# Optimization experiments

Measured on AMD Instinct MI355X. Metric: run time of the kernel, lower is better.

The kernel has to match this reference:

```python
import jax, jax.numpy as jnp
import numpy as np

NEIGHBOR_K = 3

def setup_inputs() -> dict:
    key = jax.random.key(0)
    k1, k2 = jax.random.split(key)
    query_fea = jax.random.normal(k1, (8, 75, 121, 640), dtype=jnp.float32)
    support_fea = jax.random.normal(k2, (8, 5, 5, 121, 640), dtype=jnp.float32)
    return {"query_fea": query_fea, "support_fea": support_fea}

def reference(query_fea, support_fea):
    # query_fea: [b, n_wq, patch_num, dim]
    # support_fea: [b, way, shot, patch_num, dim]
    b, way, shot, pn, dim = support_fea.shape
    sup = support_fea.reshape(b, way, shot * pn, dim)  # [b, way, S, dim]
    # inner products between every query patch and every support patch
    # sim: [b, n_wq, way, patch_num, S]
    sim = jnp.einsum('bqpd,bwsd->bqwps', query_fea, sup)
    # top-k over support patches (last axis), then mean over all topk values
    topk = jax.lax.top_k(sim, NEIGHBOR_K)[0]  # [b, n_wq, way, patch_num, k]
    return jnp.mean(topk, axis=(-2, -1))  # [b, n_wq, way]
```

## Files before the change

kernel.cpp:

```cpp
#include <hip/hip_runtime.h>
#include <hip/hip_bf16.h>

#define BATCH 8
#define NQ    75
#define WAY   5
#define PN    121
#define DIM   640
#define SSZ   605
#define TOPK  3

#define KCH 10
#define NCH 5

#define NQTILES 6000
#define NSTILES 2000
#define WSQ_BYTES ((size_t)NQTILES * 16384)
#define WS_NEED   ((size_t)(NQTILES + NSTILES) * 16384)

typedef __attribute__((ext_vector_type(8))) short   short8;
typedef __attribute__((ext_vector_type(8))) __bf16  bf16x8;
typedef __attribute__((ext_vector_type(4))) float   f32x4;

__device__ inline unsigned short f2bf(float f) {
  unsigned u = __builtin_bit_cast(unsigned, f);
  return (unsigned short)((u + 0x7fffu + ((u >> 16) & 1u)) >> 16);
}
__device__ inline unsigned pk2(float lo, float hi) {
  return (unsigned)f2bf(lo) | ((unsigned)f2bf(hi) << 16);
}

__device__ inline void ins3(float &a, float &b, float &c, float v) {
  float na  = fmaxf(a, v);
  float nb  = __builtin_amdgcn_fmed3f(v, a, b);
  float nc2 = __builtin_amdgcn_fmed3f(v, b, c);
  a = na; b = nb; c = nc2;
}

__device__ inline void async_copy16(const void* g, void* l) {
  __builtin_amdgcn_global_load_lds(
      (const __attribute__((address_space(1))) unsigned int*)g,
      (__attribute__((address_space(3))) unsigned int*)l, 16, 0, 0);
}

__global__ __launch_bounds__(256) void cvt_pack(const float* __restrict__ qf,
                                                const float* __restrict__ sf,
                                                uint4* __restrict__ wq,
                                                uint4* __restrict__ wsp) {
  const int blk = blockIdx.x;
  const float* src;
  uint4* dstbase;
  int nrows;
  int rowbase;
  if (blk < 1200) {
    const int slab = blk >> 1;
    rowbase = (blk & 1) << 6;
    src = qf + (size_t)slab * PN * DIM;
    dstbase = wq + (size_t)slab * KCH * 1024;
    nrows = PN;
  } else {
    const int u  = blk - 1200;
    const int uv = u >> 1;
    rowbase = (u & 1) << 6;
    const int nc = uv % NCH;
    const int bw = uv / NCH;
    src = sf + ((size_t)bw * SSZ + nc * 128) * DIM;
    dstbase = wsp + (size_t)uv * KCH * 1024;
    nrows = SSZ - nc * 128; if (nrows > 128) nrows = 128;
  }
  #pragma unroll 4
  for (int i = 0; i < 20; ++i) {
    const int L    = i * 256 + threadIdx.x;
    const int rowl = L / 80;
    const int s    = L - rowl * 80;
    const int row  = rowbase + rowl;
    const int kc   = s >> 3;
    const int c    = s & 7;
    const int p    = c ^ (row & 7);
    uint4 o = make_uint4(0u, 0u, 0u, 0u);
    if (row < nrows) {
      const float* g = src + (size_t)row * DIM + s * 8;
      float4 v0 = reinterpret_cast<const float4*>(g)[0];
      float4 v1 = reinterpret_cast<const float4*>(g)[1];
      o.x = pk2(v0.x, v0.y); o.y = pk2(v0.z, v0.w);
      o.z = pk2(v1.x, v1.y); o.w = pk2(v1.z, v1.w);
    }
    dstbase[(size_t)kc * 1024 + row * 8 + p] = o;
  }
}

__global__ __launch_bounds__(256, 3) void lpc_main(
    const char* __restrict__ wq,
    const char* __restrict__ wsp,
    float* __restrict__ out)
{
  __shared__ char Qs[16384];
  __shared__ char Ss[16384];
  __shared__ float red[4];

  const int sbid = blockIdx.x;
  const int bid  = (sbid & 7) * (NQ * WAY) + (sbid >> 3);

  const int w   = bid % WAY;
  const int bq  = bid / WAY;
  const int b   = bid / (WAY * NQ);

  const char* Qtiles = wq  + (size_t)bq * KCH * 16384;
  const char* Stiles = wsp + (size_t)(b * WAY + w) * NCH * KCH * 16384;

  const int tid  = threadIdx.x;
  const int lane = tid & 63;
  const int wv   = tid >> 6;
  const int l15  = lane & 15;
  const int quad = lane >> 4;
  const int mrow0 = (wv >> 1) * 64;
  const int ncol0 = (wv & 1) * 64;

  const int sw16 = (l15 & 7) * 16;
  const int cp0  = (quad * 16) ^ sw16;
  const int cp1  = ((4 + quad) * 16) ^ sw16;

  const char* qb = Qs + (mrow0 + l15) * 128;
  const char* sb = Ss + (ncol0 + l15) * 128;

  float t3a[4][4], t3b[4][4], t3c[4][4];
  #pragma unroll
  for (int mt = 0; mt < 4; ++mt)
    #pragma unroll
    for (int r = 0; r < 4; ++r) {
      t3a[mt][r] = -3.0e38f; t3b[mt][r] = -3.0e38f; t3c[mt][r] = -3.0e38f;
    }

  for (int nc = 0; nc < NCH; ++nc) {
    f32x4 acc[4][4];
    #pragma unroll
    for (int mt = 0; mt < 4; ++mt)
      #pragma unroll
      for (int nt = 0; nt < 4; ++nt)
        acc[mt][nt] = (f32x4){0.f, 0.f, 0.f, 0.f};

    #pragma unroll 1
    for (int kc = 0; kc < KCH; ++kc) {
      __syncthreads();
      {
        const char* qsl = Qtiles + (size_t)kc * 16384;
        const char* ssl = Stiles + ((size_t)nc * KCH + kc) * 16384;
        #pragma unroll
        for (int i = 0; i < 4; ++i) {
          int ch = wv * 4 + i;
          async_copy16(qsl + ch * 1024 + lane * 16, Qs + ch * 1024);
          async_copy16(ssl + ch * 1024 + lane * 16, Ss + ch * 1024);
        }
      }
      __syncthreads();

      #pragma unroll
      for (int kk = 0; kk < 2; ++kk) {
        const int cp = kk ? cp1 : cp0;
        short8 a[4], bf[4];
        #pragma unroll
        for (int mt = 0; mt < 4; ++mt)
          a[mt] = *reinterpret_cast<const short8*>(qb + mt * 2048 + cp);
        #pragma unroll
        for (int nt = 0; nt < 4; ++nt)
          bf[nt] = *reinterpret_cast<const short8*>(sb + nt * 2048 + cp);
        #pragma unroll
        for (int mt = 0; mt < 4; ++mt)
          #pragma unroll
          for (int nt = 0; nt < 4; ++nt)
            acc[mt][nt] = __builtin_amdgcn_mfma_f32_16x16x32_bf16(
                __builtin_bit_cast(bf16x8, a[mt]),
                __builtin_bit_cast(bf16x8, bf[nt]), acc[mt][nt], 0, 0, 0);
      }
    }

    #pragma unroll
    for (int nt = 0; nt < 4; ++nt) {
      int col = nc * 128 + ncol0 + nt * 16 + l15;
      bool valid = col < SSZ;
      #pragma unroll
      for (int mt = 0; mt < 4; ++mt)
        #pragma unroll
        for (int r = 0; r < 4; ++r) {
          float v = valid ? acc[mt][nt][r] : -3.0e38f;
          ins3(t3a[mt][r], t3b[mt][r], t3c[mt][r], v);
        }
    }
  }

  #pragma unroll
  for (int m = 1; m < 16; m <<= 1) {
    #pragma unroll
    for (int mt = 0; mt < 4; ++mt)
      #pragma unroll
      for (int r = 0; r < 4; ++r) {
        float o0 = __shfl_xor(t3a[mt][r], m);
        float o1 = __shfl_xor(t3b[mt][r], m);
        float o2 = __shfl_xor(t3c[mt][r], m);
        ins3(t3a[mt][r], t3b[mt][r], t3c[mt][r], o0);
        ins3(t3a[mt][r], t3b[mt][r], t3c[mt][r], o1);
        ins3(t3a[mt][r], t3b[mt][r], t3c[mt][r], o2);
      }
  }

  float* tb = reinterpret_cast<float*>(Qs);
  __syncthreads();
  if ((wv & 1) == 1 && l15 == 0) {
    #pragma unroll
    for (int mt = 0; mt < 4; ++mt)
      #pragma unroll
      for (int r = 0; r < 4; ++r) {
        int row = mrow0 + mt * 16 + quad * 4 + r;
        tb[row * 3 + 0] = t3a[mt][r];
        tb[row * 3 + 1] = t3b[mt][r];
        tb[row * 3 + 2] = t3c[mt][r];
      }
  }
  __syncthreads();
  if ((wv & 1) == 0 && l15 == 0) {
    #pragma unroll
    for (int mt = 0; mt < 4; ++mt)
      #pragma unroll
      for (int r = 0; r < 4; ++r) {
        int row = mrow0 + mt * 16 + quad * 4 + r;
        ins3(t3a[mt][r], t3b[mt][r], t3c[mt][r], tb[row * 3 + 0]);
        ins3(t3a[mt][r], t3b[mt][r], t3c[mt][r], tb[row * 3 + 1]);
        ins3(t3a[mt][r], t3b[mt][r], t3c[mt][r], tb[row * 3 + 2]);
      }
  }
  __syncthreads();
  if ((wv & 1) == 0 && l15 == 0) {
    #pragma unroll
    for (int mt = 0; mt < 4; ++mt)
      #pragma unroll
      for (int r = 0; r < 4; ++r) {
        int row = mrow0 + mt * 16 + quad * 4 + r;
        tb[row * 3 + 0] = t3a[mt][r];
        tb[row * 3 + 1] = t3b[mt][r];
        tb[row * 3 + 2] = t3c[mt][r];
      }
  }
  __syncthreads();

  float s = 0.f;
  for (int i = tid; i < PN * TOPK; i += 256) s += tb[i];
  #pragma unroll
  for (int off = 32; off > 0; off >>= 1) s += __shfl_down(s, off);
  if (lane == 0) red[wv] = s;
  __syncthreads();
  if (tid == 0)
    out[bid] = (red[0] + red[1] + red[2] + red[3]) * (1.0f / (PN * TOPK));
}

__global__ __launch_bounds__(256) void lpc_fallback(
    const float* __restrict__ qf, const float* __restrict__ sf,
    float* __restrict__ out)
{
  __shared__ short Qst[128][72];
  __shared__ short Sst[64][72];
  __shared__ float Cs[128][67];
  __shared__ float top3[128][TOPK];
  __shared__ float red[4];

  const int bid = blockIdx.x;
  const int w   = bid % WAY;
  const int qi  = (bid / WAY) % NQ;
  const int b   = bid / (WAY * NQ);
  const float* Qb = qf + ((size_t)(b * NQ + qi)) * PN * DIM;
  const float* Sb = sf + ((size_t)(b * WAY + w)) * SSZ * DIM;
  const int tid  = threadIdx.x;
  const int lane = tid & 63;
  const int wv   = tid >> 6;
  const int l15  = lane & 15;
  const int quad = lane >> 4;

  if (tid < 128) { top3[tid][0] = -3.0e38f; top3[tid][1] = -3.0e38f; top3[tid][2] = -3.0e38f; }
  f32x4 acc[2][4];
  for (int nc = 0; nc < 10; ++nc) {
    const int sbase = nc * 64;
    int vn = SSZ - sbase; if (vn > 64) vn = 64;
    #pragma unroll
    for (int mt = 0; mt < 2; ++mt)
      #pragma unroll
      for (int nt = 0; nt < 4; ++nt) acc[mt][nt] = (f32x4){0.f,0.f,0.f,0.f};
    for (int kc = 0; kc < KCH; ++kc) {
      const int kbase = kc * 64;
      __syncthreads();
      #pragma unroll
      for (int i = 0; i < 8; ++i) {
        int lin = i * 256 + tid; int row = lin >> 4; int c4 = lin & 15;
        float4 v = make_float4(0.f,0.f,0.f,0.f);
        if (row < PN) v = *reinterpret_cast<const float4*>(Qb + (size_t)row * DIM + kbase + c4 * 4);
        ushort4 h; h.x=f2bf(v.x); h.y=f2bf(v.y); h.z=f2bf(v.z); h.w=f2bf(v.w);
        *reinterpret_cast<ushort4*>(&Qst[row][c4*4]) = h;
      }
      #pragma unroll
      for (int i = 0; i < 4; ++i) {
        int lin = i * 256 + tid; int row = lin >> 4; int c4 = lin & 15;
        int srow = sbase + row;
        float4 v = make_float4(0.f,0.f,0.f,0.f);
        if (srow < SSZ) v = *reinterpret_cast<const float4*>(Sb + (size_t)srow * DIM + kbase + c4 * 4);
        ushort4 h; h.x=f2bf(v.x); h.y=f2bf(v.y); h.z=f2bf(v.z); h.w=f2bf(v.w);
        *reinterpret_cast<ushort4*>(&Sst[row][c4*4]) = h;
      }
      __syncthreads();
      #pragma unroll
      for (int kk = 0; kk < 2; ++kk) {
        bf16x8 a0 = __builtin_bit_cast(bf16x8, *reinterpret_cast<const short8*>(&Qst[wv*32+ 0+l15][kk*32+quad*8]));
        bf16x8 a1 = __builtin_bit_cast(bf16x8, *reinterpret_cast<const short8*>(&Qst[wv*32+16+l15][kk*32+quad*8]));
        #pragma unroll
        for (int nt = 0; nt < 4; ++nt) {
          bf16x8 bb = __builtin_bit_cast(bf16x8, *reinterpret_cast<const short8*>(&Sst[nt*16+l15][kk*32+quad*8]));
          acc[0][nt] = __builtin_amdgcn_mfma_f32_16x16x32_bf16(a0, bb, acc[0][nt], 0,0,0);
          acc[1][nt] = __builtin_amdgcn_mfma_f32_16x16x32_bf16(a1, bb, acc[1][nt], 0,0,0);
        }
      }
    }
    #pragma unroll
    for (int mt = 0; mt < 2; ++mt)
      #pragma unroll
      for (int nt = 0; nt < 4; ++nt)
        #pragma unroll
        for (int r = 0; r < 4; ++r)
          Cs[wv*32+mt*16+quad*4+r][nt*16+l15] = acc[mt][nt][r];
    __syncthreads();
    {
      int row = tid >> 1; int half = tid & 1;
      float a = -3.0e38f, b2 = -3.0e38f, c = -3.0e38f;
      int c0 = half * 32; int cend = c0 + 32; if (cend > vn) cend = vn;
      for (int cc = c0; cc < cend; ++cc) ins3(a, b2, c, Cs[row][cc]);
      float o0 = __shfl_xor(a,1), o1 = __shfl_xor(b2,1), o2 = __shfl_xor(c,1);
      ins3(a,b2,c,o0); ins3(a,b2,c,o1); ins3(a,b2,c,o2);
      if (half == 0) {
        float r0=top3[row][0], r1=top3[row][1], r2=top3[row][2];
        ins3(r0,r1,r2,a); ins3(r0,r1,r2,b2); ins3(r0,r1,r2,c);
        top3[row][0]=r0; top3[row][1]=r1; top3[row][2]=r2;
      }
    }
    __syncthreads();
  }
  float s = 0.f;
  for (int i = tid; i < PN * TOPK; i += 256) s += top3[i/TOPK][i%TOPK];
  #pragma unroll
  for (int off = 32; off > 0; off >>= 1) s += __shfl_down(s, off);
  if (lane == 0) red[wv] = s;
  __syncthreads();
  if (tid == 0) out[bid] = (red[0]+red[1]+red[2]+red[3]) * (1.0f/(PN*TOPK));
}

extern "C" void kernel_launch(void* const* d_in, const int* in_sizes, int n_in,
                              void* d_out, int out_size, void* d_ws, size_t ws_size,
                              hipStream_t stream) {
  const float* qf = (const float*)d_in[0];
  const float* sf = (const float*)d_in[1];
  float* out = (float*)d_out;
  (void)in_sizes; (void)n_in; (void)out_size;

  if (ws_size >= WS_NEED && d_ws != nullptr) {
    uint4* wq  = (uint4*)d_ws;
    uint4* wsp = wq + (size_t)NQTILES * 1024;
    cvt_pack<<<1600, 256, 0, stream>>>(qf, sf, wq, wsp);
    lpc_main<<<BATCH * NQ * WAY, 256, 0, stream>>>((const char*)wq, (const char*)wsp, out);
  } else {
    lpc_fallback<<<BATCH * NQ * WAY, 256, 0, stream>>>(qf, sf, out);
  }
}
```

Measured before the change: 627.3 us.

## Fuse bf16 pack and main GEMM/top-k into one cooperative persistent kernel

Merges the conversion/packing kernel and the main similarity/top-k kernel into a single cooperative launch. A persistent grid of up to 3 blocks per CU first packs fp32 inputs to swizzled bf16 tiles, then does a grid-wide sync and loops over output blocks. The aim is to remove the second kernel launch and the inter-kernel gap. In exchange it adds a grid barrier and a persistent loop whose static block-to-work assignment may balance worse than hardware scheduling. It falls back to the two-kernel path if the cooperative launch fails.

```diff
diff --git a/kernel.cpp b/kernel.cpp
--- a/kernel.cpp
+++ b/kernel.cpp
@@ -1,5 +1,8 @@
 #include <hip/hip_runtime.h>
 #include <hip/hip_bf16.h>
+#include <hip/hip_cooperative_groups.h>
+
+namespace cg = cooperative_groups;
 
 #define BATCH 8
 #define NQ    75
@@ -14,7 +17,6 @@
 
 #define NQTILES 6000
 #define NSTILES 2000
-#define WSQ_BYTES ((size_t)NQTILES * 16384)
 #define WS_NEED   ((size_t)(NQTILES + NSTILES) * 16384)
 
 typedef __attribute__((ext_vector_type(8))) short   short8;
@@ -42,33 +44,35 @@
       (__attribute__((address_space(3))) unsigned int*)l, 16, 0, 0);
 }
 
-__global__ __launch_bounds__(256) void cvt_pack(const float* __restrict__ qf,
-                                                const float* __restrict__ sf,
-                                                uint4* __restrict__ wq,
-                                                uint4* __restrict__ wsp) {
-  const int blk = blockIdx.x;
+__device__ __forceinline__ void pack_unit(int unit_b, int j,
+                                          const float* __restrict__ qf,
+                                          const float* __restrict__ sf,
+                                          uint4* __restrict__ wq,
+                                          uint4* __restrict__ wsp) {
   const float* src;
   uint4* dstbase;
-  int nrows;
-  int rowbase;
-  if (blk < 1200) {
-    const int slab = blk >> 1;
-    rowbase = (blk & 1) << 6;
+  int nrows, rowbase;
+  if (j < 300) {
+    const int q = j >> 2;
+    rowbase = (j & 3) << 5;
+    const int slab = unit_b * NQ + q;
     src = qf + (size_t)slab * PN * DIM;
     dstbase = wq + (size_t)slab * KCH * 1024;
     nrows = PN;
   } else {
-    const int u  = blk - 1200;
-    const int uv = u >> 1;
-    rowbase = (u & 1) << 6;
-    const int nc = uv % NCH;
-    const int bw = uv / NCH;
+    const int l = j - 300;
+    rowbase = (l & 3) << 5;
+    const int fi = l >> 2;
+    const int nc = fi % NCH;
+    const int w  = fi / NCH;
+    const int bw = unit_b * WAY + w;
+    const int uv = bw * NCH + nc;
     src = sf + ((size_t)bw * SSZ + nc * 128) * DIM;
     dstbase = wsp + (size_t)uv * KCH * 1024;
     nrows = SSZ - nc * 128; if (nrows > 128) nrows = 128;
   }
-  #pragma unroll 4
-  for (int i = 0; i < 20; ++i) {
+  #pragma unroll 2
+  for (int i = 0; i < 10; ++i) {
     const int L    = i * 256 + threadIdx.x;
     const int rowl = L / 80;
     const int s    = L - rowl * 80;
@@ -88,16 +92,11 @@
   }
 }
 
-__global__ __launch_bounds__(256, 3) void lpc_main(
-    const char* __restrict__ wq,
-    const char* __restrict__ wsp,
-    float* __restrict__ out)
-{
-  __shared__ char Qs[16384];
-  __shared__ char Ss[16384];
-  __shared__ float red[4];
-
-  const int sbid = blockIdx.x;
+__device__ __forceinline__ void main_block(int sbid,
+                                           const char* __restrict__ wq,
+                                           const char* __restrict__ wsp,
+                                           float* __restrict__ out,
+                                           char* Qs, char* Ss, float* red) {
   const int bid  = (sbid & 7) * (NQ * WAY) + (sbid >> 3);
 
   const int w   = bid % WAY;
@@ -249,6 +248,54 @@
   __syncthreads();
   if (tid == 0)
     out[bid] = (red[0] + red[1] + red[2] + red[3]) * (1.0f / (PN * TOPK));
+}
+
+__global__ __launch_bounds__(256, 3) void lpc_fused(
+    const float* __restrict__ qf, const float* __restrict__ sf,
+    uint4* __restrict__ wq, uint4* __restrict__ wsp,
+    float* __restrict__ out, int nblk)
+{
+  __shared__ char Qs[16384];
+  __shared__ char Ss[16384];
+  __shared__ float red[4];
+
+  const int g  = blockIdx.x;
+  const int bb = g & 7;
+  for (int j = g >> 3; j < 400; j += (nblk >> 3))
+    pack_unit(bb, j, qf, sf, wq, wsp);
+
+  __threadfence();
+  cg::this_grid().sync();
+  __threadfence();
+
+  for (int sbid = g; sbid < BATCH * NQ * WAY; sbid += nblk)
+    main_block(sbid, (const char*)wq, (const char*)wsp, out, Qs, Ss, red);
+}
+
+__global__ __launch_bounds__(256) void cvt_pack(const float* __restrict__ qf,
+                                                const float* __restrict__ sf,
+                                                uint4* __restrict__ wq,
+                                                uint4* __restrict__ wsp) {
+  const int blk = blockIdx.x;
+  int b, j0;
+  if (blk < 1200) { const int slab = blk >> 1; b = slab / NQ;
+    j0 = (slab - b * NQ) * 4 + (blk & 1) * 2; }
+  else { const int u = blk - 1200; const int uv = u >> 1;
+    const int bw = uv / NCH; b = bw / WAY;
+    const int fi = (bw - b * WAY) * NCH + (uv % NCH);
+    j0 = 300 + fi * 4 + (u & 1) * 2; }
+  pack_unit(b, j0, qf, sf, wq, wsp);
+  pack_unit(b, j0 + 1, qf, sf, wq, wsp);
+}
+
+__global__ __launch_bounds__(256, 3) void lpc_main(
+    const char* __restrict__ wq, const char* __restrict__ wsp,
+    float* __restrict__ out)
+{
+  __shared__ char Qs[16384];
+  __shared__ char Ss[16384];
+  __shared__ float red[4];
+  main_block(blockIdx.x, wq, wsp, out, Qs, Ss, red);
 }
 
 __global__ __launch_bounds__(256) void lpc_fallback(
@@ -358,8 +405,29 @@
   if (ws_size >= WS_NEED && d_ws != nullptr) {
     uint4* wq  = (uint4*)d_ws;
     uint4* wsp = wq + (size_t)NQTILES * 1024;
-    cvt_pack<<<1600, 256, 0, stream>>>(qf, sf, wq, wsp);
-    lpc_main<<<BATCH * NQ * WAY, 256, 0, stream>>>((const char*)wq, (const char*)wsp, out);
+
+    static int occ = -2;
+    if (occ == -2) {
+      int n = 0;
+      if (hipOccupancyMaxActiveBlocksPerMultiprocessor(&n, lpc_fused, 256, 0)
+          != hipSuccess) n = 0;
+      occ = n;
+    }
+
+    bool done = false;
+    if (occ >= 1) {
+      int bpc  = occ > 3 ? 3 : occ;
+      int nblk = bpc * 256;
+      void* kargs[] = { (void*)&qf, (void*)&sf, (void*)&wq, (void*)&wsp,
+                        (void*)&out, (void*)&nblk };
+      if (hipLaunchCooperativeKernel((const void*)lpc_fused, dim3(nblk),
+                                     dim3(256), kargs, 0, stream) == hipSuccess)
+        done = true;
+    }
+    if (!done) {
+      cvt_pack<<<1600, 256, 0, stream>>>(qf, sf, wq, wsp);
+      lpc_main<<<BATCH * NQ * WAY, 256, 0, stream>>>((const char*)wq, (const char*)wsp, out);
+    }
   } else {
     lpc_fallback<<<BATCH * NQ * WAY, 256, 0, stream>>>(qf, sf, out);
   }
```

New measurement: 1.097 ms. +74.9%, slower.

## Process two queries per block with double-buffered LDS staging

Applied to the files above, without the earlier changes.

The main kernel now uses 512-thread blocks that compute two query slabs against the same support tiles. Each support tile is loaded once and reused for both queries. The K/N loops are flattened into one loop with double-buffered LDS, so the next tile is prefetched while the current one feeds the MFMAs, and there is one barrier per step instead of two. The pack kernel is reorganised into per-unit helpers. In exchange, LDS per block grows to 96KB, which likely limits occupancy to one block per CU. For the odd last query the second slot reads a padding slab inside the workspace and its output write is skipped.

```diff
diff --git a/kernel.cpp b/kernel.cpp
--- a/kernel.cpp
+++ b/kernel.cpp
@@ -14,7 +14,6 @@
 
 #define NQTILES 6000
 #define NSTILES 2000
-#define WSQ_BYTES ((size_t)NQTILES * 16384)
 #define WS_NEED   ((size_t)(NQTILES + NSTILES) * 16384)
 
 typedef __attribute__((ext_vector_type(8))) short   short8;
@@ -42,33 +41,35 @@
       (__attribute__((address_space(3))) unsigned int*)l, 16, 0, 0);
 }
 
-__global__ __launch_bounds__(256) void cvt_pack(const float* __restrict__ qf,
-                                                const float* __restrict__ sf,
-                                                uint4* __restrict__ wq,
-                                                uint4* __restrict__ wsp) {
-  const int blk = blockIdx.x;
+__device__ __forceinline__ void pack_unit(int unit_b, int j,
+                                          const float* __restrict__ qf,
+                                          const float* __restrict__ sf,
+                                          uint4* __restrict__ wq,
+                                          uint4* __restrict__ wsp) {
   const float* src;
   uint4* dstbase;
-  int nrows;
-  int rowbase;
-  if (blk < 1200) {
-    const int slab = blk >> 1;
-    rowbase = (blk & 1) << 6;
+  int nrows, rowbase;
+  if (j < 300) {
+    const int q = j >> 2;
+    rowbase = (j & 3) << 5;
+    const int slab = unit_b * NQ + q;
     src = qf + (size_t)slab * PN * DIM;
     dstbase = wq + (size_t)slab * KCH * 1024;
     nrows = PN;
   } else {
-    const int u  = blk - 1200;
-    const int uv = u >> 1;
-    rowbase = (u & 1) << 6;
-    const int nc = uv % NCH;
-    const int bw = uv / NCH;
+    const int l = j - 300;
+    rowbase = (l & 3) << 5;
+    const int fi = l >> 2;
+    const int nc = fi % NCH;
+    const int w  = fi / NCH;
+    const int bw = unit_b * WAY + w;
+    const int uv = bw * NCH + nc;
     src = sf + ((size_t)bw * SSZ + nc * 128) * DIM;
     dstbase = wsp + (size_t)uv * KCH * 1024;
     nrows = SSZ - nc * 128; if (nrows > 128) nrows = 128;
   }
-  #pragma unroll 4
-  for (int i = 0; i < 20; ++i) {
+  #pragma unroll 2
+  for (int i = 0; i < 10; ++i) {
     const int L    = i * 256 + threadIdx.x;
     const int rowl = L / 80;
     const int s    = L - rowl * 80;
@@ -88,24 +89,41 @@
   }
 }
 
-__global__ __launch_bounds__(256, 3) void lpc_main(
+__global__ __launch_bounds__(256) void cvt_pack(const float* __restrict__ qf,
+                                                const float* __restrict__ sf,
+                                                uint4* __restrict__ wq,
+                                                uint4* __restrict__ wsp) {
+  const int blk = blockIdx.x;
+  int b, j0;
+  if (blk < 1200) { const int slab = blk >> 1; b = slab / NQ;
+    j0 = (slab - b * NQ) * 4 + (blk & 1) * 2; }
+  else { const int u = blk - 1200; const int uv = u >> 1;
+    const int bw = uv / NCH; b = bw / WAY;
+    const int fi = (bw - b * WAY) * NCH + (uv % NCH);
+    j0 = 300 + fi * 4 + (u & 1) * 2; }
+  pack_unit(b, j0, qf, sf, wq, wsp);
+  pack_unit(b, j0 + 1, qf, sf, wq, wsp);
+}
+
+__global__ __launch_bounds__(512, 2) void lpc_main(
     const char* __restrict__ wq,
     const char* __restrict__ wsp,
     float* __restrict__ out)
 {
-  __shared__ char Qs[16384];
-  __shared__ char Ss[16384];
-  __shared__ float red[4];
+  __shared__ char As[2][32768];
+  __shared__ char Bs[2][16384];
+  __shared__ float red[8];
 
   const int sbid = blockIdx.x;
-  const int bid  = (sbid & 7) * (NQ * WAY) + (sbid >> 3);
-
-  const int w   = bid % WAY;
-  const int bq  = bid / WAY;
-  const int b   = bid / (WAY * NQ);
-
-  const char* Qtiles = wq  + (size_t)bq * KCH * 16384;
-  const char* Stiles = wsp + (size_t)(b * WAY + w) * NCH * KCH * 16384;
+  const int b    = sbid & 7;
+  const int bid2 = sbid >> 3;
+  const int w    = bid2 % WAY;
+  const int qp   = bid2 / WAY;
+  const int q0   = qp * 2;
+
+  const char* Qt0 = wq + (size_t)(b * NQ + q0) * KCH * 16384;
+  const char* Qt1 = Qt0 + (size_t)KCH * 16384;
+  const char* St  = wsp + (size_t)(b * WAY + w) * NCH * KCH * 16384;
 
   const int tid  = threadIdx.x;
   const int lane = tid & 63;
@@ -119,8 +137,21 @@
   const int cp0  = (quad * 16) ^ sw16;
   const int cp1  = ((4 + quad) * 16) ^ sw16;
 
-  const char* qb = Qs + (mrow0 + l15) * 128;
-  const char* sb = Ss + (ncol0 + l15) * 128;
+  auto stage = [&](int buf, int tt, int kcc) {
+    const char* a0 = Qt0 + (size_t)kcc * 16384;
+    const char* a1 = Qt1 + (size_t)kcc * 16384;
+    const char* bb = St  + (size_t)tt  * 16384;
+    #pragma unroll
+    for (int i = 0; i < 6; ++i) {
+      const int c = wv * 6 + i;
+      const char* src = (c < 16) ? a0 + c * 1024
+                      : (c < 32) ? a1 + (c - 16) * 1024
+                                 : bb + (c - 32) * 1024;
+      char* dst = (c < 32) ? &As[buf][0] + c * 1024
+                           : &Bs[buf][0] + (c - 32) * 1024;
+      async_copy16(src + lane * 16, dst);
+    }
+  };
 
   float t3a[4][4], t3b[4][4], t3c[4][4];
   #pragma unroll
@@ -130,61 +161,68 @@
       t3a[mt][r] = -3.0e38f; t3b[mt][r] = -3.0e38f; t3c[mt][r] = -3.0e38f;
     }
 
-  for (int nc = 0; nc < NCH; ++nc) {
-    f32x4 acc[4][4];
-    #pragma unroll
-    for (int mt = 0; mt < 4; ++mt)
-      #pragma unroll
-      for (int nt = 0; nt < 4; ++nt)
-        acc[mt][nt] = (f32x4){0.f, 0.f, 0.f, 0.f};
-
-    #pragma unroll 1
-    for (int kc = 0; kc < KCH; ++kc) {
-      __syncthreads();
-      {
-        const char* qsl = Qtiles + (size_t)kc * 16384;
-        const char* ssl = Stiles + ((size_t)nc * KCH + kc) * 16384;
-        #pragma unroll
-        for (int i = 0; i < 4; ++i) {
-          int ch = wv * 4 + i;
-          async_copy16(qsl + ch * 1024 + lane * 16, Qs + ch * 1024);
-          async_copy16(ssl + ch * 1024 + lane * 16, Ss + ch * 1024);
-        }
-      }
-      __syncthreads();
-
-      #pragma unroll
-      for (int kk = 0; kk < 2; ++kk) {
-        const int cp = kk ? cp1 : cp0;
-        short8 a[4], bf[4];
-        #pragma unroll
-        for (int mt = 0; mt < 4; ++mt)
-          a[mt] = *reinterpret_cast<const short8*>(qb + mt * 2048 + cp);
+  stage(0, 0, 0);
+  __syncthreads();
+
+  f32x4 acc[4][4];
+  int cur = 0, kc = 0, nc = 0;
+
+  #pragma unroll 1
+  for (int t = 0; t < NCH * KCH; ++t) {
+    if (kc == 0) {
+      #pragma unroll
+      for (int mt = 0; mt < 4; ++mt)
         #pragma unroll
         for (int nt = 0; nt < 4; ++nt)
-          bf[nt] = *reinterpret_cast<const short8*>(sb + nt * 2048 + cp);
+          acc[mt][nt] = (f32x4){0.f, 0.f, 0.f, 0.f};
+    }
+
+    if (t < NCH * KCH - 1) {
+      const int kc2 = (kc == 9) ? 0 : kc + 1;
+      stage(cur ^ 1, t + 1, kc2);
+    }
+
+    const char* qb = &As[cur][0] + (mrow0 + l15) * 128;
+    const char* sb = &Bs[cur][0] + (ncol0 + l15) * 128;
+    #pragma unroll
+    for (int kk = 0; kk < 2; ++kk) {
+      const int cp = kk ? cp1 : cp0;
+      short8 a[4], bf[4];
+      #pragma unroll
+      for (int mt = 0; mt < 4; ++mt)
+        a[mt] = *reinterpret_cast<const short8*>(qb + mt * 2048 + cp);
+      #pragma unroll
+      for (int nt = 0; nt < 4; ++nt)
+        bf[nt] = *reinterpret_cast<const short8*>(sb + nt * 2048 + cp);
+      #pragma unroll
+      for (int mt = 0; mt < 4; ++mt)
+        #pragma unroll
+        for (int nt = 0; nt < 4; ++nt)
+          acc[mt][nt] = __builtin_amdgcn_mfma_f32_16x16x32_bf16(
+              __builtin_bit_cast(bf16x8, a[mt]),
+              __builtin_bit_cast(bf16x8, bf[nt]), acc[mt][nt], 0, 0, 0);
+    }
+
+    if (kc == 9) {
+      #pragma unroll
+      for (int nt = 0; nt < 4; ++nt) {
+        const int col = nc * 128 + ncol0 + nt * 16 + l15;
+        const bool valid = col < SSZ;
         #pragma unroll
         for (int mt = 0; mt < 4; ++mt)
           #pragma unroll
-          for (int nt = 0; nt < 4; ++nt)
-            acc[mt][nt] = __builtin_amdgcn_mfma_f32_16x16x32_bf16(
-                __builtin_bit_cast(bf16x8, a[mt]),
-                __builtin_bit_cast(bf16x8, bf[nt]), acc[mt][nt], 0, 0, 0);
-      }
-    }
-
-    #pragma unroll
-    for (int nt = 0; nt < 4; ++nt) {
-      int col = nc * 128 + ncol0 + nt * 16 + l15;
-      bool valid = col < SSZ;
-      #pragma unroll
-      for (int mt = 0; mt < 4; ++mt)
-        #pragma unroll
-        for (int r = 0; r < 4; ++r) {
-          float v = valid ? acc[mt][nt][r] : -3.0e38f;
-          ins3(t3a[mt][r], t3b[mt][r], t3c[mt][r], v);
-        }
-    }
+          for (int r = 0; r < 4; ++r) {
+            float v = valid ? acc[mt][nt][r] : -3.0e38f;
+            ins3(t3a[mt][r], t3b[mt][r], t3c[mt][r], v);
+          }
+      }
+      kc = 0; ++nc;
+    } else {
+      ++kc;
+    }
+
+    __syncthreads();
+    cur ^= 1;
   }
 
   #pragma unroll
@@ -202,7 +240,7 @@
       }
   }
 
-  float* tb = reinterpret_cast<float*>(Qs);
+  float* tb = reinterpret_cast<float*>(As);
   __syncthreads();
   if ((wv & 1) == 1 && l15 == 0) {
     #pragma unroll
@@ -241,14 +279,19 @@
   }
   __syncthreads();
 
+  const int half = tid >> 8;
   float s = 0.f;
-  for (int i = tid; i < PN * TOPK; i += 256) s += tb[i];
+  for (int j = tid & 255; j < PN * TOPK; j += 256) s += tb[half * 384 + j];
   #pragma unroll
   for (int off = 32; off > 0; off >>= 1) s += __shfl_down(s, off);
   if (lane == 0) red[wv] = s;
   __syncthreads();
   if (tid == 0)
-    out[bid] = (red[0] + red[1] + red[2] + red[3]) * (1.0f / (PN * TOPK));
+    out[(size_t)(b * NQ + q0) * WAY + w] =
+        (red[0] + red[1] + red[2] + red[3]) * (1.0f / (PN * TOPK));
+  if (tid == 256 && q0 + 1 < NQ)
+    out[(size_t)(b * NQ + q0 + 1) * WAY + w] =
+        (red[4] + red[5] + red[6] + red[7]) * (1.0f / (PN * TOPK));
 }
 
 __global__ __launch_bounds__(256) void lpc_fallback(
@@ -359,7 +402,8 @@
     uint4* wq  = (uint4*)d_ws;
     uint4* wsp = wq + (size_t)NQTILES * 1024;
     cvt_pack<<<1600, 256, 0, stream>>>(qf, sf, wq, wsp);
-    lpc_main<<<BATCH * NQ * WAY, 256, 0, stream>>>((const char*)wq, (const char*)wsp, out);
+    lpc_main<<<BATCH * NQ * WAY / 2 + BATCH * WAY / 2, 512, 0, stream>>>(
+        (const char*)wq, (const char*)wsp, out);
   } else {
     lpc_fallback<<<BATCH * NQ * WAY, 256, 0, stream>>>(qf, sf, out);
   }
```

After: 711.8 us. 1.13x slower.

## Load MFMA operands directly from global memory, drop LDS staging and barriers

Applied to the files above, without the earlier changes.

The main GEMM kernel stops staging Q and S tiles through shared memory with async global-to-LDS copies and two barriers per k-chunk. Each lane now reads its bf16 operand fragments straight from the pre-swizzled global workspace, which relies on L1/L2 caching instead of LDS sharing. This removes the barrier stalls and the LDS footprint, which may raise occupancy. The cost is redundant global and cache traffic, since waves sharing a tile each fetch it themselves. The pack kernel is also restructured so each block processes two smaller 32-row units per batch.

```diff
diff --git a/kernel.cpp b/kernel.cpp
--- a/kernel.cpp
+++ b/kernel.cpp
@@ -14,7 +14,6 @@
 
 #define NQTILES 6000
 #define NSTILES 2000
-#define WSQ_BYTES ((size_t)NQTILES * 16384)
 #define WS_NEED   ((size_t)(NQTILES + NSTILES) * 16384)
 
 typedef __attribute__((ext_vector_type(8))) short   short8;
@@ -36,39 +35,35 @@
   a = na; b = nb; c = nc2;
 }
 
-__device__ inline void async_copy16(const void* g, void* l) {
-  __builtin_amdgcn_global_load_lds(
-      (const __attribute__((address_space(1))) unsigned int*)g,
-      (__attribute__((address_space(3))) unsigned int*)l, 16, 0, 0);
-}
-
-__global__ __launch_bounds__(256) void cvt_pack(const float* __restrict__ qf,
-                                                const float* __restrict__ sf,
-                                                uint4* __restrict__ wq,
-                                                uint4* __restrict__ wsp) {
-  const int blk = blockIdx.x;
+__device__ __forceinline__ void pack_unit(int unit_b, int j,
+                                          const float* __restrict__ qf,
+                                          const float* __restrict__ sf,
+                                          uint4* __restrict__ wq,
+                                          uint4* __restrict__ wsp) {
   const float* src;
   uint4* dstbase;
-  int nrows;
-  int rowbase;
-  if (blk < 1200) {
-    const int slab = blk >> 1;
-    rowbase = (blk & 1) << 6;
+  int nrows, rowbase;
+  if (j < 300) {
+    const int q = j >> 2;
+    rowbase = (j & 3) << 5;
+    const int slab = unit_b * NQ + q;
     src = qf + (size_t)slab * PN * DIM;
     dstbase = wq + (size_t)slab * KCH * 1024;
     nrows = PN;
   } else {
-    const int u  = blk - 1200;
-    const int uv = u >> 1;
-    rowbase = (u & 1) << 6;
-    const int nc = uv % NCH;
-    const int bw = uv / NCH;
+    const int l = j - 300;
+    rowbase = (l & 3) << 5;
+    const int fi = l >> 2;
+    const int nc = fi % NCH;
+    const int w  = fi / NCH;
+    const int bw = unit_b * WAY + w;
+    const int uv = bw * NCH + nc;
     src = sf + ((size_t)bw * SSZ + nc * 128) * DIM;
     dstbase = wsp + (size_t)uv * KCH * 1024;
     nrows = SSZ - nc * 128; if (nrows > 128) nrows = 128;
   }
-  #pragma unroll 4
-  for (int i = 0; i < 20; ++i) {
+  #pragma unroll 2
+  for (int i = 0; i < 10; ++i) {
     const int L    = i * 256 + threadIdx.x;
     const int rowl = L / 80;
     const int s    = L - rowl * 80;
@@ -88,13 +83,28 @@
   }
 }
 
+__global__ __launch_bounds__(256) void cvt_pack(const float* __restrict__ qf,
+                                                const float* __restrict__ sf,
+                                                uint4* __restrict__ wq,
+                                                uint4* __restrict__ wsp) {
+  const int blk = blockIdx.x;
+  int b, j0;
+  if (blk < 1200) { const int slab = blk >> 1; b = slab / NQ;
+    j0 = (slab - b * NQ) * 4 + (blk & 1) * 2; }
+  else { const int u = blk - 1200; const int uv = u >> 1;
+    const int bw = uv / NCH; b = bw / WAY;
+    const int fi = (bw - b * WAY) * NCH + (uv % NCH);
+    j0 = 300 + fi * 4 + (u & 1) * 2; }
+  pack_unit(b, j0, qf, sf, wq, wsp);
+  pack_unit(b, j0 + 1, qf, sf, wq, wsp);
+}
+
 __global__ __launch_bounds__(256, 3) void lpc_main(
     const char* __restrict__ wq,
     const char* __restrict__ wsp,
     float* __restrict__ out)
 {
-  __shared__ char Qs[16384];
-  __shared__ char Ss[16384];
+  __shared__ float tb[128 * TOPK];
   __shared__ float red[4];
 
   const int sbid = blockIdx.x;
@@ -118,9 +128,10 @@
   const int sw16 = (l15 & 7) * 16;
   const int cp0  = (quad * 16) ^ sw16;
   const int cp1  = ((4 + quad) * 16) ^ sw16;
-
-  const char* qb = Qs + (mrow0 + l15) * 128;
-  const char* sb = Ss + (ncol0 + l15) * 128;
+  const unsigned aoff0 = (unsigned)((mrow0 + l15) * 128 + cp0);
+  const unsigned aoff1 = (unsigned)((mrow0 + l15) * 128 + cp1);
+  const unsigned boff0 = (unsigned)((ncol0 + l15) * 128 + cp0);
+  const unsigned boff1 = (unsigned)((ncol0 + l15) * 128 + cp1);
 
   float t3a[4][4], t3b[4][4], t3c[4][4];
   #pragma unroll
@@ -140,29 +151,33 @@
 
     #pragma unroll 1
     for (int kc = 0; kc < KCH; ++kc) {
-      __syncthreads();
+      const char* qt = Qtiles + (size_t)kc * 16384;
+      const char* st = Stiles + ((size_t)nc * KCH + kc) * 16384;
+
       {
-        const char* qsl = Qtiles + (size_t)kc * 16384;
-        const char* ssl = Stiles + ((size_t)nc * KCH + kc) * 16384;
-        #pragma unroll
-        for (int i = 0; i < 4; ++i) {
-          int ch = wv * 4 + i;
-          async_copy16(qsl + ch * 1024 + lane * 16, Qs + ch * 1024);
-          async_copy16(ssl + ch * 1024 + lane * 16, Ss + ch * 1024);
-        }
-      }
-      __syncthreads();
-
-      #pragma unroll
-      for (int kk = 0; kk < 2; ++kk) {
-        const int cp = kk ? cp1 : cp0;
         short8 a[4], bf[4];
         #pragma unroll
         for (int mt = 0; mt < 4; ++mt)
-          a[mt] = *reinterpret_cast<const short8*>(qb + mt * 2048 + cp);
+          a[mt] = *reinterpret_cast<const short8*>(qt + aoff0 + mt * 2048u);
         #pragma unroll
         for (int nt = 0; nt < 4; ++nt)
-          bf[nt] = *reinterpret_cast<const short8*>(sb + nt * 2048 + cp);
+          bf[nt] = *reinterpret_cast<const short8*>(st + boff0 + nt * 2048u);
+        #pragma unroll
+        for (int mt = 0; mt < 4; ++mt)
+          #pragma unroll
+          for (int nt = 0; nt < 4; ++nt)
+            acc[mt][nt] = __builtin_amdgcn_mfma_f32_16x16x32_bf16(
+                __builtin_bit_cast(bf16x8, a[mt]),
+                __builtin_bit_cast(bf16x8, bf[nt]), acc[mt][nt], 0, 0, 0);
+      }
+      {
+        short8 a[4], bf[4];
+        #pragma unroll
+        for (int mt = 0; mt < 4; ++mt)
+          a[mt] = *reinterpret_cast<const short8*>(qt + aoff1 + mt * 2048u);
+        #pragma unroll
+        for (int nt = 0; nt < 4; ++nt)
+          bf[nt] = *reinterpret_cast<const short8*>(st + boff1 + nt * 2048u);
         #pragma unroll
         for (int mt = 0; mt < 4; ++mt)
           #pragma unroll
@@ -202,7 +217,6 @@
       }
   }
 
-  float* tb = reinterpret_cast<float*>(Qs);
   __syncthreads();
   if ((wv & 1) == 1 && l15 == 0) {
     #pragma unroll
```

Measured after the change: 865.6 us. 1.38x slower.
